# Optimization experiments

Hardware: AMD Instinct MI355X
Metric: run time of the kernel (lower is better)

## Reference

```python
import jax, jax.numpy as jnp
import numpy as np

CH = 16        # channel_n
HID = 128      # hidden_size
IN_CH = 3      # input_channels (locked each step)
FIRE_RATE = 0.5


def _dwconv3x3(x, w, b):
    # depthwise 3x3, reflect padding (torch padding_mode='reflect', padding=1)
    xp = jnp.pad(x, ((0, 0), (0, 0), (1, 1), (1, 1)), mode='reflect')
    y = jax.lax.conv_general_dilated(
        xp, w, window_strides=(1, 1), padding='VALID',
        dimension_numbers=('NCHW', 'OIHW', 'NCHW'), feature_group_count=CH)
    return y + b[None, :, None, None]


def _conv1x1(x, w, b=None):
    # w: (out_ch, in_ch) -- squeezed 1x1 conv kernel
    y = jnp.einsum('bchw,oc->bohw', x, w)
    return y if b is None else y + b[None, :, None, None]


def setup_inputs() -> dict:
    key = jax.random.key(0)
    ks = jax.random.split(key, 8)
    B, H, W = 4, 256, 256
    x = jax.random.normal(ks[0], (B, CH, H, W), dtype=jnp.float32)
    # depthwise kernels: (CH, 1, 3, 3)
    p0_w = jax.random.normal(ks[1], (CH, 1, 3, 3), dtype=jnp.float32) * (1.0 / 3.0)
    p0_b = jax.random.normal(ks[2], (CH,), dtype=jnp.float32) * 0.1
    p1_w = jax.random.normal(ks[3], (CH, 1, 3, 3), dtype=jnp.float32) * (1.0 / 3.0)
    p1_b = jax.random.normal(ks[4], (CH,), dtype=jnp.float32) * 0.1
    # fc0: Conv2d(3*CH -> HID, k=1); fc1: Conv2d(HID -> CH, k=1, bias=False)
    fc0_w = jax.random.normal(ks[5], (HID, 3 * CH), dtype=jnp.float32) * (1.0 / np.sqrt(3 * CH))
    fc0_b = jax.random.normal(ks[6], (HID,), dtype=jnp.float32) * 0.1
    # NOTE: torch zero-inits fc1; we use small random weights so the reference is non-trivial.
    fc1_w = jax.random.normal(ks[7], (CH, HID), dtype=jnp.float32) * (0.1 / np.sqrt(HID))
    return {"x": x, "p0_w": p0_w, "p0_b": p0_b, "p1_w": p1_w, "p1_b": p1_b,
            "fc0_w": fc0_w, "fc0_b": fc0_b, "fc1_w": fc1_w, "steps": 32}


def reference(x, p0_w, p0_b, p1_w, p1_b, fc0_w, fc0_b, fc1_w, steps):
    B, _, H, W = x.shape
    input_image = x[:, :IN_CH]  # clone of input channels, re-written each step
    keys = jax.random.split(jax.random.key(42), steps)

    @jax.checkpoint
    def step(x, key):
        # perceive: depthwise 3x3 x2, concat with state
        z1 = _dwconv3x3(x, p0_w, p0_b)
        z2 = _dwconv3x3(x, p1_w, p1_b)
        y = jnp.concatenate([x, z1, z2], axis=1)        # [B, 3*CH, H, W]
        # 1x1-conv MLP
        dx = jax.nn.relu(_conv1x1(y, fc0_w, fc0_b))      # [B, HID, H, W]
        dx = _conv1x1(dx, fc1_w)                         # [B, CH, H, W]
        # stochastic fire mask: rand > fire_rate, broadcast over channels
        mask = (jax.random.uniform(key, (B, 1, H, W), dtype=x.dtype) > FIRE_RATE).astype(x.dtype)
        x = x + dx * mask                                # residual update
        x = x.at[:, :IN_CH].set(input_image)             # channel lock
        return x, None

    x, _ = jax.lax.scan(step, x, keys)
    out = x[:, 3]  # segmentation channel
    return out, x
```

## Files before the change

kernel.cpp:

```cpp
#include <hip/hip_runtime.h>
#include <cstdint>

#define CH     16
#define HPIX   256
#define WPIX   256
#define BATCH  4
#define HID    128
#define STEPS  32
#define PLANE  (HPIX * WPIX)
#define MASK_N (BATCH * PLANE)

#define TW 16
#define TH 8
#define XTW 18
#define XTH 10
#define NPX (XTH * XTW)
#define HSF 20

typedef _Float16 half8  __attribute__((ext_vector_type(8)));
typedef _Float16 half4e __attribute__((ext_vector_type(4)));
typedef float floatx4  __attribute__((ext_vector_type(4)));
typedef float floatx16 __attribute__((ext_vector_type(16)));

__host__ __device__ static inline void tf2x32(uint32_t k0, uint32_t k1,
                                              uint32_t x0, uint32_t x1,
                                              uint32_t& o0, uint32_t& o1) {
  const uint32_t ks2 = k0 ^ k1 ^ 0x1BD11BDAu;
#define TFROT(a) { x0 += x1; x1 = (x1 << (a)) | (x1 >> (32 - (a))); x1 ^= x0; }
  x0 += k0;  x1 += k1;
  TFROT(13) TFROT(15) TFROT(26) TFROT(6)
  x0 += k1;  x1 += ks2 + 1u;
  TFROT(17) TFROT(29) TFROT(16) TFROT(24)
  x0 += ks2; x1 += k0 + 2u;
  TFROT(13) TFROT(15) TFROT(26) TFROT(6)
  x0 += k0;  x1 += k1 + 3u;
  TFROT(17) TFROT(29) TFROT(16) TFROT(24)
  x0 += k1;  x1 += ks2 + 4u;
  TFROT(13) TFROT(15) TFROT(26) TFROT(6)
  x0 += ks2; x1 += k0 + 5u;
#undef TFROT
  o0 = x0; o1 = x1;
}

__global__ __launch_bounds__(256) void prep_weights(
    const float* __restrict__ fc0_w, const float* __restrict__ fc0_b,
    const float* __restrict__ fc1_w,
    const float* __restrict__ p0_w, const float* __restrict__ p0_b,
    const float* __restrict__ p1_w, const float* __restrict__ p1_b,
    _Float16* __restrict__ Mh, _Float16* __restrict__ W1h,
    float* __restrict__ bp) {
  const int idx = blockIdx.x * 256 + threadIdx.x;
  if (idx < 9 * HID * CH) {
    const int tap = idx / (HID * CH);
    const int rem = idx - tap * (HID * CH);
    const int h = rem >> 4, c = rem & 15;
    float m = fc0_w[h * 48 + 16 + c] * p0_w[c * 9 + tap]
            + fc0_w[h * 48 + 32 + c] * p1_w[c * 9 + tap];
    if (tap == 4) m += fc0_w[h * 48 + c];
    Mh[(tap * HID + h) * CH + c] = (_Float16)m;
  } else if (idx < 9 * HID * CH + CH * HID) {
    const int i2 = idx - 9 * HID * CH;
    W1h[i2] = (_Float16)fc1_w[i2];
  } else if (idx < 9 * HID * CH + CH * HID + HID) {
    const int h = idx - (9 * HID * CH + CH * HID);
    float s = fc0_b[h];
    for (int c = 0; c < CH; ++c)
      s += fc0_w[h * 48 + 16 + c] * p0_b[c]
         + fc0_w[h * 48 + 32 + c] * p1_b[c];
    bp[h] = s;
  }
}

__global__ __launch_bounds__(256) void nca_step(
    const float* __restrict__ x_in, float* __restrict__ x_out,
    const _Float16* __restrict__ Mh, const _Float16* __restrict__ W1h,
    const float* __restrict__ bp,
    uint32_t k0, uint32_t k1) {
  __shared__ __align__(16) _Float16 halo[NPX * HSF];
  __shared__ __align__(16) _Float16 Hbuf[128 * HID];
  __shared__ float maskbuf[128];

  const int tid = threadIdx.x;
  const int w0 = blockIdx.x * TW;
  const int h0 = blockIdx.y * TH;
  const int b  = blockIdx.z;

  const int wv   = tid >> 6;
  const int lane = tid & 63;
  const int n    = lane & 15;
  const int g    = lane >> 4;
  const int c32  = lane & 31;
  const int q2   = lane >> 5;

  half8 Atap[9];
  #pragma unroll
  for (int t = 0; t < 9; ++t)
    Atap[t] = *(const half8*)(Mh + ((t * HID + 32 * wv + c32) << 4) + 8 * q2);
  half8 bw1[4];
  #pragma unroll
  for (int s = 0; s < 4; ++s)
    bw1[s] = *(const half8*)(W1h + n * HID + 32 * s + 8 * g);
  float4 bias4[4];
  #pragma unroll
  for (int rb = 0; rb < 4; ++rb)
    bias4[rb] = *(const float4*)(bp + 32 * wv + 8 * rb + 4 * q2);

  const float* __restrict__ xb = x_in + (size_t)b * CH * PLANE;

  if (tid < NPX) {
    const int hr = tid / XTW, hc = tid - (tid / XTW) * XTW;
    int gh = h0 + hr - 1;
    gh = (gh < 0) ? -gh : ((gh > HPIX - 1) ? (2 * (HPIX - 1) - gh) : gh);
    int gw = w0 + hc - 1;
    gw = (gw < 0) ? -gw : ((gw > WPIX - 1) ? (2 * (WPIX - 1) - gw) : gw);
    const float* __restrict__ src = xb + gh * WPIX + gw;
    #pragma unroll
    for (int blk = 0; blk < 4; ++blk) {
      half4e h4;
      #pragma unroll
      for (int e = 0; e < 4; ++e)
        h4[e] = (_Float16)src[(size_t)(4 * blk + e) * PLANE];
      *(half4e*)(halo + tid * HSF + 4 * blk) = h4;
    }
  }

  if (lane < 32) {
    const int pxl = wv * 32 + lane;
    const int hp = h0 + (pxl >> 4), wp = w0 + (pxl & 15);
    const uint32_t j = (uint32_t)(b * PLANE + hp * WPIX + wp);
    uint32_t r0, r1;
    tf2x32(k0, k1, 0u, j, r0, r1);
    const uint32_t bits = r0 ^ r1;
    union { uint32_t i; float f; } cvt;
    cvt.i = (bits >> 9) | 0x3F800000u;
    maskbuf[pxl] = ((cvt.f - 1.0f) > 0.5f) ? 1.0f : 0.0f;
  }
  __syncthreads();

  #pragma unroll
  for (int ct = 0; ct < 4; ++ct) {
    const int prow = 2 * ct + (c32 >> 4);
    const int pcol = c32 & 15;
    half8 btap[9];
    #pragma unroll
    for (int dr = 0; dr < 3; ++dr) {
      #pragma unroll
      for (int dj = 0; dj < 3; ++dj) {
        const _Float16* hp = halo + ((prow + dr) * XTW + pcol + dj) * HSF + 8 * q2;
        const half4e lo = *(const half4e*)hp;
        const half4e hi = *(const half4e*)(hp + 4);
        half8 f;
        f[0] = lo[0]; f[1] = lo[1]; f[2] = lo[2]; f[3] = lo[3];
        f[4] = hi[0]; f[5] = hi[1]; f[6] = hi[2]; f[7] = hi[3];
        btap[dr * 3 + dj] = f;
      }
    }
    floatx16 acc = {0.f,0.f,0.f,0.f,0.f,0.f,0.f,0.f,
                    0.f,0.f,0.f,0.f,0.f,0.f,0.f,0.f};
    #pragma unroll
    for (int t = 0; t < 9; ++t)
      acc = __builtin_amdgcn_mfma_f32_32x32x16_f16(Atap[t], btap[t], acc, 0, 0, 0);

    const int px  = 32 * ct + c32;
    const int n16 = px & 15;
    #pragma unroll
    for (int rb = 0; rb < 4; ++rb) {
      half4e hv;
      hv[0] = (_Float16)fmaxf(acc[4 * rb + 0] + bias4[rb].x, 0.f);
      hv[1] = (_Float16)fmaxf(acc[4 * rb + 1] + bias4[rb].y, 0.f);
      hv[2] = (_Float16)fmaxf(acc[4 * rb + 2] + bias4[rb].z, 0.f);
      hv[3] = (_Float16)fmaxf(acc[4 * rb + 3] + bias4[rb].w, 0.f);
      *(half4e*)(Hbuf + px * HID + (((4 * wv + rb) ^ n16) << 3) + 4 * q2) = hv;
    }
  }
  __syncthreads();

  float* __restrict__ xob = x_out + (size_t)b * CH * PLANE;
  #pragma unroll
  for (int i = 0; i < 2; ++i) {
    const int ct2 = 2 * wv + i;
    floatx4 c2 = {0.f, 0.f, 0.f, 0.f};
    #pragma unroll
    for (int ks = 0; ks < 4; ++ks) {
      const half8 a2 =
          *(const half8*)(Hbuf + (16 * ct2 + n) * HID + (((4 * ks + g) ^ n) << 3));
      c2 = __builtin_amdgcn_mfma_f32_16x16x32_f16(a2, bw1[ks], c2, 0, 0, 0);
    }
    const float4 mk = *(const float4*)(maskbuf + 16 * ct2 + 4 * g);
    const size_t off = (size_t)n * PLANE + (size_t)(h0 + ct2) * WPIX + w0 + 4 * g;
    const float4 xc = *(const float4*)(xb + off);
    float4 res;
    res.x = (n < 3) ? xc.x : fmaf(mk.x, c2[0], xc.x);
    res.y = (n < 3) ? xc.y : fmaf(mk.y, c2[1], xc.y);
    res.z = (n < 3) ? xc.z : fmaf(mk.z, c2[2], xc.z);
    res.w = (n < 3) ? xc.w : fmaf(mk.w, c2[3], xc.w);
    *(float4*)(xob + off) = res;
  }
}

__global__ __launch_bounds__(256) void extract_ch3(
    const float* __restrict__ xf, float* __restrict__ out) {
  const int i = blockIdx.x * 256 + threadIdx.x;
  if (i >= MASK_N) return;
  const int b = i >> 16;
  const int p = i & (PLANE - 1);
  out[i] = xf[((size_t)b * CH + 3) * PLANE + p];
}

extern "C" void kernel_launch(void* const* d_in, const int* in_sizes, int n_in,
                              void* d_out, int out_size, void* d_ws, size_t ws_size,
                              hipStream_t stream) {
  const float* x     = (const float*)d_in[0];
  const float* p0_w  = (const float*)d_in[1];
  const float* p0_b  = (const float*)d_in[2];
  const float* p1_w  = (const float*)d_in[3];
  const float* p1_b  = (const float*)d_in[4];
  const float* fc0_w = (const float*)d_in[5];
  const float* fc0_b = (const float*)d_in[6];
  const float* fc1_w = (const float*)d_in[7];

  uint32_t kk[STEPS][2];
  for (int i = 0; i < STEPS; ++i) {
    uint32_t a, b2;
    tf2x32(0u, 42u, 0u, (uint32_t)i, a, b2);
    kk[i][0] = a;
    kk[i][1] = b2;
  }

  float* out = (float*)d_out;
  _Float16* Mh  = (_Float16*)d_out;
  _Float16* W1h = Mh + 9 * HID * CH;
  float*    bpr = (float*)((char*)d_out + (9 * HID * CH + CH * HID) * 2);
  float* bufA = out + MASK_N;
  float* bufB = (float*)d_ws;

  const int prep_n = 9 * HID * CH + CH * HID + HID;
  prep_weights<<<dim3((prep_n + 255) / 256), dim3(256), 0, stream>>>(
      fc0_w, fc0_b, fc1_w, p0_w, p0_b, p1_w, p1_b, Mh, W1h, bpr);

  const dim3 grid(WPIX / TW, HPIX / TH, BATCH);
  const dim3 block(256);

  for (int i = 0; i < STEPS; ++i) {
    const float* src = (i == 0) ? x : ((i & 1) ? bufB : bufA);
    float* dst = (i & 1) ? bufA : bufB;
    nca_step<<<grid, block, 0, stream>>>(src, dst, Mh, W1h, bpr,
                                         kk[i][0], kk[i][1]);
  }
  extract_ch3<<<dim3(MASK_N / 256), dim3(256), 0, stream>>>(bufA, out);
}
```

Baseline: 749.9 us.

## Halve hidden LDS buffer, prefetch residual, skip locked-channel writes

Splits the hidden-activation stage into two halves so the LDS buffer shrinks from 128 to 64 pixel rows, which may allow more resident blocks per CU. The residual x values are prefetched at kernel start to hide global latency. The three locked input channels are read from the original input and are written only on the final step, which saves global stores. The trade is an extra barrier per half and reads of locked channels from a second buffer.

Result: faster. 733.4 us (-2.2%).

```diff
diff --git a/kernel.cpp b/kernel.cpp
--- a/kernel.cpp
+++ b/kernel.cpp
@@ -73,11 +73,12 @@
 
 __global__ __launch_bounds__(256) void nca_step(
     const float* __restrict__ x_in, float* __restrict__ x_out,
+    const float* __restrict__ x0,
     const _Float16* __restrict__ Mh, const _Float16* __restrict__ W1h,
     const float* __restrict__ bp,
-    uint32_t k0, uint32_t k1) {
+    uint32_t k0, uint32_t k1, int wrgb) {
   __shared__ __align__(16) _Float16 halo[NPX * HSF];
-  __shared__ __align__(16) _Float16 Hbuf[128 * HID];
+  __shared__ __align__(16) _Float16 Hbuf[64 * HID];
   __shared__ float maskbuf[128];
 
   const int tid = threadIdx.x;
@@ -92,6 +93,9 @@
   const int c32  = lane & 31;
   const int q2   = lane >> 5;
 
+  const float* __restrict__ xb  = x_in + (size_t)b * CH * PLANE;
+  const float* __restrict__ x0b = x0   + (size_t)b * CH * PLANE;
+
   half8 Atap[9];
   #pragma unroll
   for (int t = 0; t < 9; ++t)
@@ -105,7 +109,13 @@
   for (int rb = 0; rb < 4; ++rb)
     bias4[rb] = *(const float4*)(bp + 32 * wv + 8 * rb + 4 * q2);
 
-  const float* __restrict__ xb = x_in + (size_t)b * CH * PLANE;
+  float4 xcv[2];
+  size_t xoff[2];
+  #pragma unroll
+  for (int i = 0; i < 2; ++i) {
+    xoff[i] = (size_t)n * PLANE + (size_t)(h0 + 4 * i + wv) * WPIX + w0 + 4 * g;
+    xcv[i] = *(const float4*)(((n < 3) ? x0b : xb) + xoff[i]);
+  }
 
   if (tid < NPX) {
     const int hr = tid / XTW, hc = tid - (tid / XTW) * XTW;
@@ -113,13 +123,16 @@
     gh = (gh < 0) ? -gh : ((gh > HPIX - 1) ? (2 * (HPIX - 1) - gh) : gh);
     int gw = w0 + hc - 1;
     gw = (gw < 0) ? -gw : ((gw > WPIX - 1) ? (2 * (WPIX - 1) - gw) : gw);
-    const float* __restrict__ src = xb + gh * WPIX + gw;
+    const float* __restrict__ srcS = xb  + gh * WPIX + gw;
+    const float* __restrict__ src0 = x0b + gh * WPIX + gw;
     #pragma unroll
     for (int blk = 0; blk < 4; ++blk) {
       half4e h4;
       #pragma unroll
-      for (int e = 0; e < 4; ++e)
-        h4[e] = (_Float16)src[(size_t)(4 * blk + e) * PLANE];
+      for (int e = 0; e < 4; ++e) {
+        const int c = 4 * blk + e;
+        h4[e] = (_Float16)((c < 3 ? src0 : srcS)[(size_t)c * PLANE]);
+      }
       *(half4e*)(halo + tid * HSF + 4 * blk) = h4;
     }
   }
@@ -137,64 +150,71 @@
   }
   __syncthreads();
 
-  #pragma unroll
-  for (int ct = 0; ct < 4; ++ct) {
-    const int prow = 2 * ct + (c32 >> 4);
-    const int pcol = c32 & 15;
-    half8 btap[9];
+  float* __restrict__ xob = x_out + (size_t)b * CH * PLANE;
+
+  #pragma unroll
+  for (int half = 0; half < 2; ++half) {
     #pragma unroll
-    for (int dr = 0; dr < 3; ++dr) {
-      #pragma unroll
-      for (int dj = 0; dj < 3; ++dj) {
-        const _Float16* hp = halo + ((prow + dr) * XTW + pcol + dj) * HSF + 8 * q2;
-        const half4e lo = *(const half4e*)hp;
-        const half4e hi = *(const half4e*)(hp + 4);
-        half8 f;
-        f[0] = lo[0]; f[1] = lo[1]; f[2] = lo[2]; f[3] = lo[3];
-        f[4] = hi[0]; f[5] = hi[1]; f[6] = hi[2]; f[7] = hi[3];
-        btap[dr * 3 + dj] = f;
+    for (int cti = 0; cti < 2; ++cti) {
+      const int ct   = 2 * half + cti;
+      const int prow = 2 * ct + (c32 >> 4);
+      const int pcol = c32 & 15;
+      half8 btap[9];
+      #pragma unroll
+      for (int dr = 0; dr < 3; ++dr) {
+        #pragma unroll
+        for (int dj = 0; dj < 3; ++dj) {
+          const _Float16* hp =
+              halo + ((prow + dr) * XTW + pcol + dj) * HSF + 8 * q2;
+          const half4e lo = *(const half4e*)hp;
+          const half4e hi = *(const half4e*)(hp + 4);
+          half8 ff;
+          ff[0] = lo[0]; ff[1] = lo[1]; ff[2] = lo[2]; ff[3] = lo[3];
+          ff[4] = hi[0]; ff[5] = hi[1]; ff[6] = hi[2]; ff[7] = hi[3];
+          btap[dr * 3 + dj] = ff;
+        }
+      }
+      floatx16 acc = {0.f,0.f,0.f,0.f,0.f,0.f,0.f,0.f,
+                      0.f,0.f,0.f,0.f,0.f,0.f,0.f,0.f};
+      #pragma unroll
+      for (int t = 0; t < 9; ++t)
+        acc = __builtin_amdgcn_mfma_f32_32x32x16_f16(Atap[t], btap[t], acc,
+                                                     0, 0, 0);
+      const int px  = 32 * ct + c32;
+      const int ph  = px & 63;
+      const int n16 = px & 15;
+      #pragma unroll
+      for (int rb = 0; rb < 4; ++rb) {
+        half4e hv;
+        hv[0] = (_Float16)fmaxf(acc[4 * rb + 0] + bias4[rb].x, 0.f);
+        hv[1] = (_Float16)fmaxf(acc[4 * rb + 1] + bias4[rb].y, 0.f);
+        hv[2] = (_Float16)fmaxf(acc[4 * rb + 2] + bias4[rb].z, 0.f);
+        hv[3] = (_Float16)fmaxf(acc[4 * rb + 3] + bias4[rb].w, 0.f);
+        *(half4e*)(Hbuf + ph * HID + (((4 * wv + rb) ^ n16) << 3) + 4 * q2) = hv;
       }
     }
-    floatx16 acc = {0.f,0.f,0.f,0.f,0.f,0.f,0.f,0.f,
-                    0.f,0.f,0.f,0.f,0.f,0.f,0.f,0.f};
-    #pragma unroll
-    for (int t = 0; t < 9; ++t)
-      acc = __builtin_amdgcn_mfma_f32_32x32x16_f16(Atap[t], btap[t], acc, 0, 0, 0);
-
-    const int px  = 32 * ct + c32;
-    const int n16 = px & 15;
-    #pragma unroll
-    for (int rb = 0; rb < 4; ++rb) {
-      half4e hv;
-      hv[0] = (_Float16)fmaxf(acc[4 * rb + 0] + bias4[rb].x, 0.f);
-      hv[1] = (_Float16)fmaxf(acc[4 * rb + 1] + bias4[rb].y, 0.f);
-      hv[2] = (_Float16)fmaxf(acc[4 * rb + 2] + bias4[rb].z, 0.f);
-      hv[3] = (_Float16)fmaxf(acc[4 * rb + 3] + bias4[rb].w, 0.f);
-      *(half4e*)(Hbuf + px * HID + (((4 * wv + rb) ^ n16) << 3) + 4 * q2) = hv;
+    __syncthreads();
+
+    {
+      const int ct2 = 4 * half + wv;
+      floatx4 c2 = {0.f, 0.f, 0.f, 0.f};
+      #pragma unroll
+      for (int ks = 0; ks < 4; ++ks) {
+        const half8 a2 = *(const half8*)(
+            Hbuf + (16 * (ct2 & 3) + n) * HID + (((4 * ks + g) ^ n) << 3));
+        c2 = __builtin_amdgcn_mfma_f32_16x16x32_f16(a2, bw1[ks], c2, 0, 0, 0);
+      }
+      const float4 mk = *(const float4*)(maskbuf + 16 * ct2 + 4 * g);
+      const float4 xc = xcv[half];
+      float4 res;
+      res.x = (n < 3) ? xc.x : fmaf(mk.x, c2[0], xc.x);
+      res.y = (n < 3) ? xc.y : fmaf(mk.y, c2[1], xc.y);
+      res.z = (n < 3) ? xc.z : fmaf(mk.z, c2[2], xc.z);
+      res.w = (n < 3) ? xc.w : fmaf(mk.w, c2[3], xc.w);
+      if (n >= 3 || wrgb)
+        *(float4*)(xob + xoff[half]) = res;
     }
-  }
-  __syncthreads();
-
-  float* __restrict__ xob = x_out + (size_t)b * CH * PLANE;
-  #pragma unroll
-  for (int i = 0; i < 2; ++i) {
-    const int ct2 = 2 * wv + i;
-    floatx4 c2 = {0.f, 0.f, 0.f, 0.f};
-    #pragma unroll
-    for (int ks = 0; ks < 4; ++ks) {
-      const half8 a2 =
-          *(const half8*)(Hbuf + (16 * ct2 + n) * HID + (((4 * ks + g) ^ n) << 3));
-      c2 = __builtin_amdgcn_mfma_f32_16x16x32_f16(a2, bw1[ks], c2, 0, 0, 0);
-    }
-    const float4 mk = *(const float4*)(maskbuf + 16 * ct2 + 4 * g);
-    const size_t off = (size_t)n * PLANE + (size_t)(h0 + ct2) * WPIX + w0 + 4 * g;
-    const float4 xc = *(const float4*)(xb + off);
-    float4 res;
-    res.x = (n < 3) ? xc.x : fmaf(mk.x, c2[0], xc.x);
-    res.y = (n < 3) ? xc.y : fmaf(mk.y, c2[1], xc.y);
-    res.z = (n < 3) ? xc.z : fmaf(mk.z, c2[2], xc.z);
-    res.w = (n < 3) ? xc.w : fmaf(mk.w, c2[3], xc.w);
-    *(float4*)(xob + off) = res;
+    if (half == 0) __syncthreads();
   }
 }
 
@@ -244,8 +264,9 @@
   for (int i = 0; i < STEPS; ++i) {
     const float* src = (i == 0) ? x : ((i & 1) ? bufB : bufA);
     float* dst = (i & 1) ? bufA : bufB;
-    nca_step<<<grid, block, 0, stream>>>(src, dst, Mh, W1h, bpr,
-                                         kk[i][0], kk[i][1]);
+    nca_step<<<grid, block, 0, stream>>>(src, dst, x, Mh, W1h, bpr,
+                                         kk[i][0], kk[i][1],
+                                         (i == STEPS - 1) ? 1 : 0);
   }
   extract_ch3<<<dim3(MASK_N / 256), dim3(256), 0, stream>>>(bufA, out);
 }
```
